# Kernel optimization log

Measured on AMD Instinct MI355X. Metric: run time of the kernel, lower is better.

Reference implementation:

```python
import jax, jax.numpy as jnp
import numpy as np

N = 170000      # nodes (ogbn-arxiv scale)
E = 2720000     # edges (avg degree 16)
IN, H, L, OUT = 128, 256, 4, 40
BN_EPS = 1e-5


def setup_inputs() -> dict:
    key = jax.random.key(0)
    ks = jax.random.split(key, 6)
    x = jax.random.normal(ks[0], (N, IN), jnp.float32)
    edge_index = jax.random.randint(ks[1], (2, E), 0, N, dtype=jnp.int64)
    W_in = jax.random.normal(ks[2], (IN, H), jnp.float32) * 0.05
    b_in = jnp.zeros((H,), jnp.float32)
    W_hid = jax.random.normal(ks[3], (L - 1, H, H), jnp.float32) * 0.05
    b_hid = jnp.zeros((L - 1, H), jnp.float32)
    gamma = jnp.ones((L, H), jnp.float32)
    beta = jnp.zeros((L, H), jnp.float32)
    W_out = jax.random.normal(ks[4], (L * H, OUT), jnp.float32) * 0.05
    b_out = jnp.zeros((OUT,), jnp.float32)
    return dict(x=x, edge_index=edge_index, W_in=W_in, b_in=b_in,
                W_hid=W_hid, b_hid=b_hid, gamma=gamma, beta=beta,
                W_out=W_out, b_out=b_out)


def _gcn_aggregate(h, src, dst, norm_e, inv_deg):
    # message passing with symmetric normalization + self-loop term
    msg = h[src] * norm_e[:, None]                      # [E, H] gather
    agg = jax.ops.segment_sum(msg, dst, num_segments=N)  # [N, H] scatter-add
    return agg + h * inv_deg[:, None]                   # self-loop: deg^-1


def reference(x, edge_index, W_in, b_in, W_hid, b_hid, gamma, beta, W_out, b_out):
    src, dst = edge_index[0], edge_index[1]
    # degree (incl. self-loop), PyG gcn_norm style
    deg = jax.ops.segment_sum(jnp.ones((E,), x.dtype), dst, num_segments=N) + 1.0
    dinv = jax.lax.rsqrt(deg)
    norm_e = dinv[src] * dinv[dst]
    inv_deg = 1.0 / deg

    outs = []
    h = x
    for i in range(L):
        W = W_in if i == 0 else W_hid[i - 1]
        b = b_in if i == 0 else b_hid[i - 1]
        h = _gcn_aggregate(h @ W, src, dst, norm_e, inv_deg) + b
        # BatchNorm1d (training-mode batch statistics, biased variance)
        mean = jnp.mean(h, axis=0)
        var = jnp.mean(jnp.square(h - mean), axis=0)
        h = (h - mean) * jax.lax.rsqrt(var + BN_EPS) * gamma[i] + beta[i]
        h = jax.nn.relu(h)  # dropout is identity in eval mode
        outs.append(h)

    z = jnp.concatenate(outs, axis=-1) @ W_out + b_out  # JK 'cat' -> [N, L*H] @ [L*H, OUT]
    return jax.nn.log_softmax(z, axis=-1)
```

## Files before the change

### kernel.cpp

```cpp
#include <hip/hip_runtime.h>
#include <math.h>

constexpr int kN = 170000;
constexpr int kE = 2720000;
constexpr int kFin = 128;
constexpr int kFh = 256;
constexpr int kL = 4;
constexpr int kFout = 40;

typedef __attribute__((ext_vector_type(8))) short bf16x8;
typedef __attribute__((ext_vector_type(4))) float f32x4;

__device__ __forceinline__ float jk_b2f(unsigned short u) {
    unsigned int x = ((unsigned int)u) << 16;
    float f;
    __builtin_memcpy(&f, &x, 4);
    return f;
}
__device__ __forceinline__ unsigned short jk_f2b(float f) {
    unsigned int x;
    __builtin_memcpy(&x, &f, 4);
    unsigned int r = (x + 0x7fffu + ((x >> 16) & 1u)) >> 16;
    return (unsigned short)r;
}

union U4 {
    uint4 v;
    unsigned short s[8];
};
union U2 {
    uint2 v;
    unsigned short s[4];
};

__global__ void jk8_zero_i(int* p, int n) {
    int i = blockIdx.x * blockDim.x + threadIdx.x;
    if (i < n) p[i] = 0;
}
__global__ void jk8_zero_f(float* p, int n) {
    int i = blockIdx.x * blockDim.x + threadIdx.x;
    if (i < n) p[i] = 0.0f;
}

__global__ void jk8_detect(const int* eb, int* flag) {
    __shared__ int nz;
    if (threadIdx.x == 0) nz = 0;
    __syncthreads();
    int bad = 0;
    for (int j = 0; j < 4; j++) {
        int idx = threadIdx.x * 4 + j;
        if (eb[2 * idx + 1] != 0) bad = 1;
    }
    if (bad) atomicOr(&nz, 1);
    __syncthreads();
    if (threadIdx.x == 0) {
        flag[0] = nz ? 0 : 1;
        flag[1] = 0;
    }
}

__global__ void jk8_count(const int* eb, const int* flag, int* counts, int* rank) {
    int e0 = (blockIdx.x * blockDim.x + threadIdx.x) * 4;
    if (e0 >= kE) return;
    int s64 = flag[0];
    int d[4];
    if (s64) {
        int4 c1 = *(const int4*)(eb + 2 * ((size_t)kE + e0));
        int4 c2 = *(const int4*)(eb + 2 * ((size_t)kE + e0) + 4);
        d[0] = c1.x; d[1] = c1.z; d[2] = c2.x; d[3] = c2.z;
    } else {
        int4 c1 = *(const int4*)(eb + (size_t)kE + e0);
        d[0] = c1.x; d[1] = c1.y; d[2] = c1.z; d[3] = c1.w;
    }
    int r[4];
#pragma unroll
    for (int q = 0; q < 4; q++) r[q] = atomicAdd(&counts[d[q]], 1);
    *(int4*)(rank + e0) = make_int4(r[0], r[1], r[2], r[3]);
}

__global__ void jk8_nodeprep(const int* counts, float* dinv, float* invdeg, int* off,
                             int* cursor) {
    int n = blockIdx.x * blockDim.x + threadIdx.x;
    if (n < kN) {
        int c = counts[n];
        float deg = (float)c + 1.0f;
        dinv[n] = rsqrtf(deg);
        invdeg[n] = 1.0f / deg;
        off[n] = atomicAdd(cursor, c);
    }
}

__global__ void jk8_fill(const int* eb, const int* flag, const int* rank, const int* off,
                         const float* dinv, int2* csr) {
    int e0 = (blockIdx.x * blockDim.x + threadIdx.x) * 4;
    if (e0 >= kE) return;
    int s64 = flag[0];
    int s[4], d[4];
    if (s64) {
        int4 a1 = *(const int4*)(eb + 2 * (size_t)e0);
        int4 a2 = *(const int4*)(eb + 2 * (size_t)e0 + 4);
        s[0] = a1.x; s[1] = a1.z; s[2] = a2.x; s[3] = a2.z;
        int4 c1 = *(const int4*)(eb + 2 * ((size_t)kE + e0));
        int4 c2 = *(const int4*)(eb + 2 * ((size_t)kE + e0) + 4);
        d[0] = c1.x; d[1] = c1.z; d[2] = c2.x; d[3] = c2.z;
    } else {
        int4 a1 = *(const int4*)(eb + (size_t)e0);
        s[0] = a1.x; s[1] = a1.y; s[2] = a1.z; s[3] = a1.w;
        int4 c1 = *(const int4*)(eb + (size_t)kE + e0);
        d[0] = c1.x; d[1] = c1.y; d[2] = c1.z; d[3] = c1.w;
    }
    int4 rr = *(const int4*)(rank + e0);
    int r[4] = {rr.x, rr.y, rr.z, rr.w};
#pragma unroll
    for (int q = 0; q < 4; q++) {
        int p = off[d[q]] + r[q];
        float w = dinv[s[q]] * dinv[d[q]];
        csr[p] = make_int2(s[q], __float_as_int(w));
    }
}

__global__ void jk8_prepw(const float* W_in, const float* W_hid, const float* Wout,
                          unsigned short* Wt0, unsigned short* Wt1, unsigned short* Wto) {
    int idx = blockIdx.x * blockDim.x + threadIdx.x;
    if (idx < 32768) {
        int c = idx >> 7, k = idx & 127;
        Wt0[idx] = jk_f2b(W_in[(size_t)k * kFh + c]);
    } else if (idx < 32768 + 196608) {
        int t2 = idx - 32768;
        int l = t2 >> 16, rem = t2 & 65535;
        int c = rem >> 8, k = rem & 255;
        Wt1[(size_t)l * 65536 + rem] = jk_f2b(W_hid[(size_t)l * 65536 + k * kFh + c]);
    } else if (idx < 32768 + 196608 + 49152) {
        int t2 = idx - 32768 - 196608;
        int l = t2 / (48 * 256), rem = t2 % (48 * 256);
        int col = rem >> 8, k = rem & 255;
        float wv = (col < kFout) ? Wout[(size_t)(l * kFh + k) * kFout + col] : 0.f;
        unsigned short hi = jk_f2b(wv);
        unsigned short lo = jk_f2b(wv - jk_b2f(hi));
        Wto[((size_t)(l * 2 + 0) * 48 + col) * 256 + k] = hi;
        Wto[((size_t)(l * 2 + 1) * 48 + col) * 256 + k] = lo;
    }
}

__global__ void jk8_xb(const float* x, unsigned short* xb) {
    int i = blockIdx.x * blockDim.x + threadIdx.x;
    if (i >= kN * kFin / 8) return;
    float4 a = *(const float4*)(x + (size_t)i * 8);
    float4 b = *(const float4*)(x + (size_t)i * 8 + 4);
    U4 o;
    o.s[0] = jk_f2b(a.x); o.s[1] = jk_f2b(a.y); o.s[2] = jk_f2b(a.z); o.s[3] = jk_f2b(a.w);
    o.s[4] = jk_f2b(b.x); o.s[5] = jk_f2b(b.y); o.s[6] = jk_f2b(b.z); o.s[7] = jk_f2b(b.w);
    *(uint4*)(xb + (size_t)i * 8) = o.v;
}

template <int MODE>
__global__ __launch_bounds__(256) void jk8_gemm(const unsigned short* A, const unsigned short* Wt,
                                                unsigned short* C, int K, const float* sc,
                                                const float* sh, const float* bias) {
    __shared__ unsigned short As[128][40];
    __shared__ unsigned short Bs[128][40];
    __shared__ float ssc[256], ssh[256];
    int tid = threadIdx.x;
    if (MODE == 1) {
        ssc[tid] = sc[tid];
        ssh[tid] = sh[tid];
    } else {
        ssc[tid] = bias[tid];
    }
    __syncthreads();
    int row0 = blockIdx.x * 128;
    int n0 = blockIdx.y * 128;
    int lane = tid & 63, w = tid >> 6;
    int wm = w >> 1, wn = w & 1;
    int lr = lane & 15, lg = lane >> 4;

    f32x4 acc[4][4];
#pragma unroll
    for (int i = 0; i < 4; i++)
#pragma unroll
        for (int j = 0; j < 4; j++) acc[i][j] = (f32x4){0.f, 0.f, 0.f, 0.f};

    int sr = tid >> 1;
    int skh = (tid & 1) * 16;

    for (int k0 = 0; k0 < K; k0 += 32) {
        {
            int row = row0 + sr;
            if (MODE == 0) {
                uint4 u0 = make_uint4(0, 0, 0, 0), u1 = make_uint4(0, 0, 0, 0);
                if (row < kN) {
                    const unsigned short* g = A + (size_t)row * K + k0 + skh;
                    u0 = *(const uint4*)g;
                    u1 = *(const uint4*)(g + 8);
                }
                *(uint4*)&As[sr][skh] = u0;
                *(uint4*)&As[sr][skh + 8] = u1;
            } else {
                U4 o0, o1;
                if (row < kN) {
                    U4 u0, u1;
                    const unsigned short* g = A + (size_t)row * K + k0 + skh;
                    u0.v = *(const uint4*)g;
                    u1.v = *(const uint4*)(g + 8);
#pragma unroll
                    for (int j = 0; j < 8; j++) {
                        float v = jk_b2f(u0.s[j]) * ssc[k0 + skh + j] + ssh[k0 + skh + j];
                        o0.s[j] = jk_f2b(v > 0.f ? v : 0.f);
                    }
#pragma unroll
                    for (int j = 0; j < 8; j++) {
                        float v = jk_b2f(u1.s[j]) * ssc[k0 + skh + 8 + j] + ssh[k0 + skh + 8 + j];
                        o1.s[j] = jk_f2b(v > 0.f ? v : 0.f);
                    }
                } else {
#pragma unroll
                    for (int j = 0; j < 8; j++) { o0.s[j] = 0; o1.s[j] = 0; }
                }
                *(uint4*)&As[sr][skh] = o0.v;
                *(uint4*)&As[sr][skh + 8] = o1.v;
            }
        }
        {
            const unsigned short* g = Wt + (size_t)(n0 + sr) * K + k0 + skh;
            *(uint4*)&Bs[sr][skh] = *(const uint4*)g;
            *(uint4*)&Bs[sr][skh + 8] = *(const uint4*)(g + 8);
        }
        __syncthreads();

        bf16x8 af[4], bfr[4];
#pragma unroll
        for (int mi = 0; mi < 4; mi++)
            af[mi] = *(const bf16x8*)&As[wm * 64 + mi * 16 + lr][lg * 8];
#pragma unroll
        for (int ni = 0; ni < 4; ni++)
            bfr[ni] = *(const bf16x8*)&Bs[wn * 64 + ni * 16 + lr][lg * 8];
#pragma unroll
        for (int mi = 0; mi < 4; mi++)
#pragma unroll
            for (int ni = 0; ni < 4; ni++)
                acc[mi][ni] = __builtin_amdgcn_mfma_f32_16x16x32_bf16(af[mi], bfr[ni],
                                                                      acc[mi][ni], 0, 0, 0);
        __syncthreads();
    }

#pragma unroll
    for (int mi = 0; mi < 4; mi++) {
#pragma unroll
        for (int j = 0; j < 4; j++) {
            int row = row0 + wm * 64 + mi * 16 + lg * 4 + j;
            if (row < kN) {
#pragma unroll
                for (int ni = 0; ni < 4; ni++) {
                    int col = n0 + wn * 64 + ni * 16 + lr;
                    float v = acc[mi][ni][j];
                    if (MODE == 0) v += ssc[col];
                    C[(size_t)row * kFh + col] = jk_f2b(v);
                }
            }
        }
    }
}

template <int CH, int HASB>
__global__ __launch_bounds__(256) void jk8_agg(const unsigned short* t, const float* bias,
                                               const int* off, const int* cnt, const int2* csr,
                                               const float* invdeg, unsigned short* h) {
    constexpr int PC = CH / 32;
    constexpr int DEPTH = (CH == 128) ? 8 : 6;
    int n = blockIdx.x * 8 + (threadIdx.x >> 5);
    if (n >= kN) return;
    int c0 = (threadIdx.x & 31) * PC;

    float acc[PC];
    {
        float sw = invdeg[n];
        if constexpr (PC == 8) {
            U4 u;
            u.v = *(const uint4*)(t + (size_t)n * CH + c0);
#pragma unroll
            for (int j = 0; j < 8; j++) acc[j] = sw * jk_b2f(u.s[j]);
        } else {
            U2 u;
            u.v = *(const uint2*)(t + (size_t)n * CH + c0);
#pragma unroll
            for (int j = 0; j < 4; j++) acc[j] = sw * jk_b2f(u.s[j]);
        }
    }

    int base = off[n], c = cnt[n];
    for (int i = 0; i < c; i += DEPTH) {
        float w[DEPTH];
        U4 u8[PC == 8 ? DEPTH : 1];
        U2 u4[PC == 4 ? DEPTH : 1];
#pragma unroll
        for (int q = 0; q < DEPTH; q++) {
            int e = i + q;
            bool v = e < c;
            int2 cw = csr[v ? base + e : base];
            w[q] = v ? __int_as_float(cw.y) : 0.0f;
            if constexpr (PC == 8)
                u8[q].v = *(const uint4*)(t + (size_t)cw.x * CH + c0);
            else
                u4[q].v = *(const uint2*)(t + (size_t)cw.x * CH + c0);
        }
#pragma unroll
        for (int q = 0; q < DEPTH; q++) {
            if constexpr (PC == 8) {
#pragma unroll
                for (int j = 0; j < 8; j++) acc[j] += w[q] * jk_b2f(u8[q].s[j]);
            } else {
#pragma unroll
                for (int j = 0; j < 4; j++) acc[j] += w[q] * jk_b2f(u4[q].s[j]);
            }
        }
    }

    if constexpr (PC == 8) {
        U4 o;
#pragma unroll
        for (int j = 0; j < 8; j++)
            o.s[j] = jk_f2b(HASB ? acc[j] + bias[c0 + j] : acc[j]);
        *(uint4*)(h + (size_t)n * CH + c0) = o.v;
    } else {
        U2 o;
#pragma unroll
        for (int j = 0; j < 4; j++)
            o.s[j] = jk_f2b(HASB ? acc[j] + bias[c0 + j] : acc[j]);
        *(uint2*)(h + (size_t)n * CH + c0) = o.v;
    }
}

__global__ __launch_bounds__(256) void jk8_bnstats(const unsigned short* h, float* stats) {
    __shared__ float lsum[256], lsq[256];
    int tid = threadIdx.x;
    lsum[tid] = 0.f;
    lsq[tid] = 0.f;
    __syncthreads();
    int c0 = (tid & 31) * 8;
    int grp = tid >> 5;
    float rs[8] = {}, rq[8] = {};
    for (int n = blockIdx.x * 8 + grp; n < kN; n += gridDim.x * 8) {
        U4 u;
        u.v = *(const uint4*)(h + (size_t)n * kFh + c0);
#pragma unroll
        for (int j = 0; j < 8; j++) {
            float v = jk_b2f(u.s[j]);
            rs[j] += v;
            rq[j] += v * v;
        }
    }
#pragma unroll
    for (int j = 0; j < 8; j++) {
        atomicAdd(&lsum[c0 + j], rs[j]);
        atomicAdd(&lsq[c0 + j], rq[j]);
    }
    __syncthreads();
    atomicAdd(&stats[tid], lsum[tid]);
    atomicAdd(&stats[256 + tid], lsq[tid]);
}

__global__ void jk8_bnfinal(const float* stats, const float* gamma, const float* beta, int layer,
                            float* scale, float* shift) {
    int c = threadIdx.x;
    float mean = stats[c] / (float)kN;
    float var = stats[256 + c] / (float)kN - mean * mean;
    var = var < 0.f ? 0.f : var;
    float sc = gamma[layer * kFh + c] * rsqrtf(var + 1e-5f);
    scale[c] = sc;
    shift[c] = beta[layer * kFh + c] - mean * sc;
}

template <int FIRST, int LAST>
__global__ __launch_bounds__(256) void jk8_zacc(const unsigned short* h, const float* scale,
                                                const float* shift, const unsigned short* Wto,
                                                const float* bout, float* z, float* out) {
    __shared__ unsigned short Bs[2][48][264];
    __shared__ unsigned short As[128][40];
    __shared__ float ssc[256], ssh[256];
    int tid = threadIdx.x;
    for (int f = tid; f < 2 * 48 * 256; f += 256) {
        int hl = f / (48 * 256);
        int rem = f % (48 * 256);
        Bs[hl][rem >> 8][rem & 255] = Wto[f];
    }
    ssc[tid] = scale[tid];
    ssh[tid] = shift[tid];
    __syncthreads();

    int row0 = blockIdx.x * 128;
    int w = tid >> 6, lane = tid & 63;
    int lr = lane & 15, lg = lane >> 4;
    int sr = tid >> 1, skh = (tid & 1) * 16;

    f32x4 acc[2][3];
#pragma unroll
    for (int mi = 0; mi < 2; mi++)
#pragma unroll
        for (int ni = 0; ni < 3; ni++) acc[mi][ni] = (f32x4){0.f, 0.f, 0.f, 0.f};

    for (int k0 = 0; k0 < kFh; k0 += 32) {
        int row = row0 + sr;
        U4 o0, o1;
        if (row < kN) {
            U4 u0, u1;
            const unsigned short* g = h + (size_t)row * kFh + k0 + skh;
            u0.v = *(const uint4*)g;
            u1.v = *(const uint4*)(g + 8);
#pragma unroll
            for (int j = 0; j < 8; j++) {
                float v = jk_b2f(u0.s[j]) * ssc[k0 + skh + j] + ssh[k0 + skh + j];
                o0.s[j] = jk_f2b(v > 0.f ? v : 0.f);
            }
#pragma unroll
            for (int j = 0; j < 8; j++) {
                float v = jk_b2f(u1.s[j]) * ssc[k0 + skh + 8 + j] + ssh[k0 + skh + 8 + j];
                o1.s[j] = jk_f2b(v > 0.f ? v : 0.f);
            }
        } else {
#pragma unroll
            for (int j = 0; j < 8; j++) { o0.s[j] = 0; o1.s[j] = 0; }
        }
        *(uint4*)&As[sr][skh] = o0.v;
        *(uint4*)&As[sr][skh + 8] = o1.v;
        __syncthreads();

        bf16x8 af[2], bh[3], bl[3];
#pragma unroll
        for (int mi = 0; mi < 2; mi++)
            af[mi] = *(const bf16x8*)&As[w * 32 + mi * 16 + lr][lg * 8];
#pragma unroll
        for (int ni = 0; ni < 3; ni++) {
            bh[ni] = *(const bf16x8*)&Bs[0][ni * 16 + lr][k0 + lg * 8];
            bl[ni] = *(const bf16x8*)&Bs[1][ni * 16 + lr][k0 + lg * 8];
        }
#pragma unroll
        for (int mi = 0; mi < 2; mi++)
#pragma unroll
            for (int ni = 0; ni < 3; ni++) {
                acc[mi][ni] = __builtin_amdgcn_mfma_f32_16x16x32_bf16(af[mi], bh[ni],
                                                                      acc[mi][ni], 0, 0, 0);
                acc[mi][ni] = __builtin_amdgcn_mfma_f32_16x16x32_bf16(af[mi], bl[ni],
                                                                      acc[mi][ni], 0, 0, 0);
            }
        __syncthreads();
    }

#pragma unroll
    for (int mi = 0; mi < 2; mi++) {
#pragma unroll
        for (int j = 0; j < 4; j++) {
            int row = row0 + w * 32 + mi * 16 + lg * 4 + j;
            if (row >= kN) continue;
            if (!LAST) {
#pragma unroll
                for (int ni = 0; ni < 3; ni++) {
                    int col = ni * 16 + lr;
                    if (col < kFout) {
                        if (FIRST)
                            z[(size_t)row * kFout + col] = acc[mi][ni][j] + bout[col];
                        else
                            z[(size_t)row * kFout + col] += acc[mi][ni][j];
                    }
                }
            } else {
                const float* zp = z + (size_t)row * kFout;
                float v0 = zp[lr] + acc[mi][0][j];
                float v1 = zp[16 + lr] + acc[mi][1][j];
                float v2 = (lr < 8) ? (zp[32 + lr] + acc[mi][2][j]) : -1e30f;
                float m = fmaxf(fmaxf(v0, v1), v2);
                m = fmaxf(m, __shfl_xor(m, 1, 64));
                m = fmaxf(m, __shfl_xor(m, 2, 64));
                m = fmaxf(m, __shfl_xor(m, 4, 64));
                m = fmaxf(m, __shfl_xor(m, 8, 64));
                float s = expf(v0 - m) + expf(v1 - m) + ((lr < 8) ? expf(v2 - m) : 0.f);
                s += __shfl_xor(s, 1, 64);
                s += __shfl_xor(s, 2, 64);
                s += __shfl_xor(s, 4, 64);
                s += __shfl_xor(s, 8, 64);
                float ls = m + logf(s);
                float* op = out + (size_t)row * kFout;
                op[lr] = v0 - ls;
                op[16 + lr] = v1 - ls;
                if (lr < 8) op[32 + lr] = v2 - ls;
            }
        }
    }
}

extern "C" void kernel_launch(void* const* d_in, const int* in_sizes, int n_in,
                              void* d_out, int out_size, void* d_ws, size_t ws_size,
                              hipStream_t stream) {
    (void)in_sizes; (void)n_in; (void)out_size; (void)ws_size;
    const float* x = (const float*)d_in[0];
    const int* eb = (const int*)d_in[1];
    const float* W_in = (const float*)d_in[2];
    const float* b_in = (const float*)d_in[3];
    const float* W_hid = (const float*)d_in[4];
    const float* b_hid = (const float*)d_in[5];
    const float* gamma = (const float*)d_in[6];
    const float* beta = (const float*)d_in[7];
    const float* W_out = (const float*)d_in[8];
    const float* b_out = (const float*)d_in[9];
    float* out = (float*)d_out;

    char* p = (char*)d_ws;
    auto alloc = [&](size_t b) -> void* {
        void* r = (void*)p;
        p += (b + 255) & ~(size_t)255;
        return r;
    };
    int* flag = (int*)alloc(8);
    int* counts = (int*)alloc((size_t)kN * 4);
    int* off = (int*)alloc((size_t)kN * 4);
    float* dinv = (float*)alloc((size_t)kN * 4);
    float* invdeg = (float*)alloc((size_t)kN * 4);
    float* bnsums = (float*)alloc((size_t)kL * 512 * 4);
    float* bnss = (float*)alloc((size_t)kL * 512 * 4);
    int* rank = (int*)alloc((size_t)kE * 4);
    int2* csr = (int2*)alloc((size_t)kE * 8);
    unsigned short* hA = (unsigned short*)alloc((size_t)kN * kFh * 2);
    unsigned short* hB = (unsigned short*)alloc((size_t)kN * kFh * 2);
    float* z = (float*)alloc((size_t)kN * kFout * 4);
    unsigned short* Wt0 = (unsigned short*)alloc((size_t)kFin * kFh * 2);
    unsigned short* Wt1 = (unsigned short*)alloc((size_t)3 * kFh * kFh * 2);
    unsigned short* Wto = (unsigned short*)alloc((size_t)kL * 2 * 48 * 256 * 2);

    jk8_zero_i<<<(kN + 255) / 256, 256, 0, stream>>>(counts, kN);
    jk8_zero_f<<<(kL * 512 + 255) / 256, 256, 0, stream>>>(bnsums, kL * 512);
    jk8_detect<<<1, 256, 0, stream>>>(eb, flag);
    jk8_count<<<(kE / 4 + 255) / 256, 256, 0, stream>>>(eb, flag, counts, rank);
    jk8_nodeprep<<<(kN + 255) / 256, 256, 0, stream>>>(counts, dinv, invdeg, off, flag + 1);
    jk8_fill<<<(kE / 4 + 255) / 256, 256, 0, stream>>>(eb, flag, rank, off, dinv, csr);
    jk8_prepw<<<(32768 + 196608 + 49152 + 255) / 256, 256, 0, stream>>>(W_in, W_hid, W_out,
                                                                        Wt0, Wt1, Wto);
    jk8_xb<<<(kN * kFin / 8 + 255) / 256, 256, 0, stream>>>(x, hB);
    jk8_agg<128, 0><<<(kN + 7) / 8, 256, 0, stream>>>(hB, nullptr, off, counts, csr, invdeg, hA);

    unsigned short* Wts[4] = {Wt0, Wt1, Wt1 + 65536, Wt1 + 131072};
    dim3 gg((kN + 127) / 128, 2);
    int zg = (kN + 127) / 128;
    for (int l = 0; l < kL; l++) {
        if (l == 0) {
            jk8_gemm<0><<<gg, 256, 0, stream>>>(hA, Wts[0], hB, kFin, nullptr, nullptr, b_in);
        } else {
            const float* b = b_hid + (size_t)(l - 1) * kFh;
            float* scp = bnss + (size_t)(l - 1) * 512;
            jk8_gemm<1><<<gg, 256, 0, stream>>>(hB, Wts[l], hA, kFh, scp, scp + 256, nullptr);
            jk8_agg<256, 1><<<(kN + 7) / 8, 256, 0, stream>>>(hA, b, off, counts, csr, invdeg,
                                                              hB);
        }
        jk8_bnstats<<<1024, 256, 0, stream>>>(hB, bnsums + (size_t)l * 512);
        jk8_bnfinal<<<1, 256, 0, stream>>>(bnsums + (size_t)l * 512, gamma, beta, l,
                                           bnss + (size_t)l * 512, bnss + (size_t)l * 512 + 256);
        const unsigned short* wtl = Wto + (size_t)l * 2 * 48 * 256;
        float* sc = bnss + (size_t)l * 512;
        if (l == 0)
            jk8_zacc<1, 0><<<zg, 256, 0, stream>>>(hB, sc, sc + 256, wtl, b_out, z, out);
        else if (l < kL - 1)
            jk8_zacc<0, 0><<<zg, 256, 0, stream>>>(hB, sc, sc + 256, wtl, b_out, z, out);
        else
            jk8_zacc<0, 1><<<zg, 256, 0, stream>>>(hB, sc, sc + 256, wtl, b_out, z, out);
    }
}
```

Baseline: 1.656 ms.

## Fuse BatchNorm statistics into GEMM and aggregation epilogues, drop bnstats pass

BatchNorm sum and sum-of-squares are now accumulated in the epilogue of the layer-0 GEMM and the hidden-layer aggregation kernels, using shared-memory atomics and then global atomics. This removes the separate bnstats kernel, which re-read the full node-feature matrix every layer. The aggregation kernel also moves to 512-thread blocks with 16 nodes per block, and its gather depth for the 256-channel case drops from 6 to 4. Statistics are now taken from the fp32 values before bf16 rounding, and the extra atomics add contention in the epilogues.

```diff
diff --git a/kernel.cpp b/kernel.cpp
--- a/kernel.cpp
+++ b/kernel.cpp
@@ -33,16 +33,16 @@
     unsigned short s[4];
 };
 
-__global__ void jk8_zero_i(int* p, int n) {
+__global__ void jk9_zero_i(int* p, int n) {
     int i = blockIdx.x * blockDim.x + threadIdx.x;
     if (i < n) p[i] = 0;
 }
-__global__ void jk8_zero_f(float* p, int n) {
+__global__ void jk9_zero_f(float* p, int n) {
     int i = blockIdx.x * blockDim.x + threadIdx.x;
     if (i < n) p[i] = 0.0f;
 }
 
-__global__ void jk8_detect(const int* eb, int* flag) {
+__global__ void jk9_detect(const int* eb, int* flag) {
     __shared__ int nz;
     if (threadIdx.x == 0) nz = 0;
     __syncthreads();
@@ -59,7 +59,7 @@
     }
 }
 
-__global__ void jk8_count(const int* eb, const int* flag, int* counts, int* rank) {
+__global__ void jk9_count(const int* eb, const int* flag, int* counts, int* rank) {
     int e0 = (blockIdx.x * blockDim.x + threadIdx.x) * 4;
     if (e0 >= kE) return;
     int s64 = flag[0];
@@ -78,7 +78,7 @@
     *(int4*)(rank + e0) = make_int4(r[0], r[1], r[2], r[3]);
 }
 
-__global__ void jk8_nodeprep(const int* counts, float* dinv, float* invdeg, int* off,
+__global__ void jk9_nodeprep(const int* counts, float* dinv, float* invdeg, int* off,
                              int* cursor) {
     int n = blockIdx.x * blockDim.x + threadIdx.x;
     if (n < kN) {
@@ -90,7 +90,7 @@
     }
 }
 
-__global__ void jk8_fill(const int* eb, const int* flag, const int* rank, const int* off,
+__global__ void jk9_fill(const int* eb, const int* flag, const int* rank, const int* off,
                          const float* dinv, int2* csr) {
     int e0 = (blockIdx.x * blockDim.x + threadIdx.x) * 4;
     if (e0 >= kE) return;
@@ -119,7 +119,7 @@
     }
 }
 
-__global__ void jk8_prepw(const float* W_in, const float* W_hid, const float* Wout,
+__global__ void jk9_prepw(const float* W_in, const float* W_hid, const float* Wout,
                           unsigned short* Wt0, unsigned short* Wt1, unsigned short* Wto) {
     int idx = blockIdx.x * blockDim.x + threadIdx.x;
     if (idx < 32768) {
@@ -142,7 +142,7 @@
     }
 }
 
-__global__ void jk8_xb(const float* x, unsigned short* xb) {
+__global__ void jk9_xb(const float* x, unsigned short* xb) {
     int i = blockIdx.x * blockDim.x + threadIdx.x;
     if (i >= kN * kFin / 8) return;
     float4 a = *(const float4*)(x + (size_t)i * 8);
@@ -154,18 +154,21 @@
 }
 
 template <int MODE>
-__global__ __launch_bounds__(256) void jk8_gemm(const unsigned short* A, const unsigned short* Wt,
+__global__ __launch_bounds__(256) void jk9_gemm(const unsigned short* A, const unsigned short* Wt,
                                                 unsigned short* C, int K, const float* sc,
-                                                const float* sh, const float* bias) {
+                                                const float* sh, const float* bias,
+                                                float* stats) {
     __shared__ unsigned short As[128][40];
     __shared__ unsigned short Bs[128][40];
     __shared__ float ssc[256], ssh[256];
+    __shared__ float csum[128], csq[128];
     int tid = threadIdx.x;
     if (MODE == 1) {
         ssc[tid] = sc[tid];
         ssh[tid] = sh[tid];
     } else {
         ssc[tid] = bias[tid];
+        if (tid < 128) { csum[tid] = 0.f; csq[tid] = 0.f; }
     }
     __syncthreads();
     int row0 = blockIdx.x * 128;
@@ -243,6 +246,7 @@
         __syncthreads();
     }
 
+    float ps[4] = {0.f, 0.f, 0.f, 0.f}, pq[4] = {0.f, 0.f, 0.f, 0.f};
 #pragma unroll
     for (int mi = 0; mi < 4; mi++) {
 #pragma unroll
@@ -253,113 +257,131 @@
                 for (int ni = 0; ni < 4; ni++) {
                     int col = n0 + wn * 64 + ni * 16 + lr;
                     float v = acc[mi][ni][j];
-                    if (MODE == 0) v += ssc[col];
+                    if (MODE == 0) {
+                        v += ssc[col];
+                        ps[ni] += v;
+                        pq[ni] += v * v;
+                    }
                     C[(size_t)row * kFh + col] = jk_f2b(v);
                 }
             }
         }
     }
-}
-
-template <int CH, int HASB>
-__global__ __launch_bounds__(256) void jk8_agg(const unsigned short* t, const float* bias,
+    if (MODE == 0) {
+#pragma unroll
+        for (int ni = 0; ni < 4; ni++) {
+            int lc = wn * 64 + ni * 16 + lr;
+            atomicAdd(&csum[lc], ps[ni]);
+            atomicAdd(&csq[lc], pq[ni]);
+        }
+        __syncthreads();
+        if (tid < 128) {
+            atomicAdd(&stats[n0 + tid], csum[tid]);
+            atomicAdd(&stats[256 + n0 + tid], csq[tid]);
+        }
+    }
+}
+
+template <int CH, int HASB, int STATS>
+__global__ __launch_bounds__(512) void jk9_agg(const unsigned short* t, const float* bias,
                                                const int* off, const int* cnt, const int2* csr,
-                                               const float* invdeg, unsigned short* h) {
+                                               const float* invdeg, unsigned short* h,
+                                               float* stats) {
     constexpr int PC = CH / 32;
-    constexpr int DEPTH = (CH == 128) ? 8 : 6;
-    int n = blockIdx.x * 8 + (threadIdx.x >> 5);
-    if (n >= kN) return;
-    int c0 = (threadIdx.x & 31) * PC;
-
-    float acc[PC];
-    {
-        float sw = invdeg[n];
+    constexpr int DEPTH = (CH == 128) ? 8 : 4;
+    __shared__ float lsum[CH], lsq[CH];
+    int tid = threadIdx.x;
+    if (STATS) {
+        if (tid < CH) {
+            lsum[tid] = 0.f;
+            lsq[tid] = 0.f;
+        }
+        __syncthreads();
+    }
+    int n = blockIdx.x * 16 + (tid >> 5);
+    bool act = n < kN;
+    int c0 = (tid & 31) * PC;
+    float vv[PC];
+
+    if (act) {
+        float acc[PC];
+        {
+            float sw = invdeg[n];
+            if constexpr (PC == 8) {
+                U4 u;
+                u.v = *(const uint4*)(t + (size_t)n * CH + c0);
+#pragma unroll
+                for (int j = 0; j < 8; j++) acc[j] = sw * jk_b2f(u.s[j]);
+            } else {
+                U2 u;
+                u.v = *(const uint2*)(t + (size_t)n * CH + c0);
+#pragma unroll
+                for (int j = 0; j < 4; j++) acc[j] = sw * jk_b2f(u.s[j]);
+            }
+        }
+        int base = off[n], c = cnt[n];
+        for (int i = 0; i < c; i += DEPTH) {
+            float w[DEPTH];
+            U4 u8[PC == 8 ? DEPTH : 1];
+            U2 u4[PC == 4 ? DEPTH : 1];
+#pragma unroll
+            for (int q = 0; q < DEPTH; q++) {
+                int e = i + q;
+                bool v = e < c;
+                int2 cw = csr[v ? base + e : base];
+                w[q] = v ? __int_as_float(cw.y) : 0.0f;
+                if constexpr (PC == 8)
+                    u8[q].v = *(const uint4*)(t + (size_t)cw.x * CH + c0);
+                else
+                    u4[q].v = *(const uint2*)(t + (size_t)cw.x * CH + c0);
+            }
+#pragma unroll
+            for (int q = 0; q < DEPTH; q++) {
+                if constexpr (PC == 8) {
+#pragma unroll
+                    for (int j = 0; j < 8; j++) acc[j] += w[q] * jk_b2f(u8[q].s[j]);
+                } else {
+#pragma unroll
+                    for (int j = 0; j < 4; j++) acc[j] += w[q] * jk_b2f(u4[q].s[j]);
+                }
+            }
+        }
         if constexpr (PC == 8) {
-            U4 u;
-            u.v = *(const uint4*)(t + (size_t)n * CH + c0);
-#pragma unroll
-            for (int j = 0; j < 8; j++) acc[j] = sw * jk_b2f(u.s[j]);
+            U4 o;
+#pragma unroll
+            for (int j = 0; j < 8; j++) {
+                vv[j] = HASB ? acc[j] + bias[c0 + j] : acc[j];
+                o.s[j] = jk_f2b(vv[j]);
+            }
+            *(uint4*)(h + (size_t)n * CH + c0) = o.v;
         } else {
-            U2 u;
-            u.v = *(const uint2*)(t + (size_t)n * CH + c0);
-#pragma unroll
-            for (int j = 0; j < 4; j++) acc[j] = sw * jk_b2f(u.s[j]);
-        }
-    }
-
-    int base = off[n], c = cnt[n];
-    for (int i = 0; i < c; i += DEPTH) {
-        float w[DEPTH];
-        U4 u8[PC == 8 ? DEPTH : 1];
-        U2 u4[PC == 4 ? DEPTH : 1];
-#pragma unroll
-        for (int q = 0; q < DEPTH; q++) {
-            int e = i + q;
-            bool v = e < c;
-            int2 cw = csr[v ? base + e : base];
-            w[q] = v ? __int_as_float(cw.y) : 0.0f;
-            if constexpr (PC == 8)
-                u8[q].v = *(const uint4*)(t + (size_t)cw.x * CH + c0);
-            else
-                u4[q].v = *(const uint2*)(t + (size_t)cw.x * CH + c0);
-        }
-#pragma unroll
-        for (int q = 0; q < DEPTH; q++) {
-            if constexpr (PC == 8) {
-#pragma unroll
-                for (int j = 0; j < 8; j++) acc[j] += w[q] * jk_b2f(u8[q].s[j]);
-            } else {
-#pragma unroll
-                for (int j = 0; j < 4; j++) acc[j] += w[q] * jk_b2f(u4[q].s[j]);
-            }
-        }
-    }
-
-    if constexpr (PC == 8) {
-        U4 o;
-#pragma unroll
-        for (int j = 0; j < 8; j++)
-            o.s[j] = jk_f2b(HASB ? acc[j] + bias[c0 + j] : acc[j]);
-        *(uint4*)(h + (size_t)n * CH + c0) = o.v;
-    } else {
-        U2 o;
-#pragma unroll
-        for (int j = 0; j < 4; j++)
-            o.s[j] = jk_f2b(HASB ? acc[j] + bias[c0 + j] : acc[j]);
-        *(uint2*)(h + (size_t)n * CH + c0) = o.v;
-    }
-}
-
-__global__ __launch_bounds__(256) void jk8_bnstats(const unsigned short* h, float* stats) {
-    __shared__ float lsum[256], lsq[256];
-    int tid = threadIdx.x;
-    lsum[tid] = 0.f;
-    lsq[tid] = 0.f;
-    __syncthreads();
-    int c0 = (tid & 31) * 8;
-    int grp = tid >> 5;
-    float rs[8] = {}, rq[8] = {};
-    for (int n = blockIdx.x * 8 + grp; n < kN; n += gridDim.x * 8) {
-        U4 u;
-        u.v = *(const uint4*)(h + (size_t)n * kFh + c0);
-#pragma unroll
-        for (int j = 0; j < 8; j++) {
-            float v = jk_b2f(u.s[j]);
-            rs[j] += v;
-            rq[j] += v * v;
-        }
-    }
-#pragma unroll
-    for (int j = 0; j < 8; j++) {
-        atomicAdd(&lsum[c0 + j], rs[j]);
-        atomicAdd(&lsq[c0 + j], rq[j]);
-    }
-    __syncthreads();
-    atomicAdd(&stats[tid], lsum[tid]);
-    atomicAdd(&stats[256 + tid], lsq[tid]);
-}
-
-__global__ void jk8_bnfinal(const float* stats, const float* gamma, const float* beta, int layer,
+            U2 o;
+#pragma unroll
+            for (int j = 0; j < 4; j++) {
+                vv[j] = HASB ? acc[j] + bias[c0 + j] : acc[j];
+                o.s[j] = jk_f2b(vv[j]);
+            }
+            *(uint2*)(h + (size_t)n * CH + c0) = o.v;
+        }
+    }
+
+    if (STATS) {
+        if (act) {
+#pragma unroll
+            for (int j = 0; j < PC; j++) {
+                atomicAdd(&lsum[c0 + j], vv[j]);
+                atomicAdd(&lsq[c0 + j], vv[j] * vv[j]);
+            }
+        }
+        __syncthreads();
+        if (tid < CH) {
+            atomicAdd(&stats[tid], lsum[tid]);
+            atomicAdd(&stats[CH + tid], lsq[tid]);
+        }
+    }
+}
+
+__global__ void jk9_bnfinal(const float* stats, const float* gamma, const float* beta, int layer,
                             float* scale, float* shift) {
     int c = threadIdx.x;
     float mean = stats[c] / (float)kN;
@@ -371,7 +393,7 @@
 }
 
 template <int FIRST, int LAST>
-__global__ __launch_bounds__(256) void jk8_zacc(const unsigned short* h, const float* scale,
+__global__ __launch_bounds__(256) void jk9_zacc(const unsigned short* h, const float* scale,
                                                 const float* shift, const unsigned short* Wto,
                                                 const float* bout, float* z, float* out) {
     __shared__ unsigned short Bs[2][48][264];
@@ -525,40 +547,43 @@
     unsigned short* Wt1 = (unsigned short*)alloc((size_t)3 * kFh * kFh * 2);
     unsigned short* Wto = (unsigned short*)alloc((size_t)kL * 2 * 48 * 256 * 2);
 
-    jk8_zero_i<<<(kN + 255) / 256, 256, 0, stream>>>(counts, kN);
-    jk8_zero_f<<<(kL * 512 + 255) / 256, 256, 0, stream>>>(bnsums, kL * 512);
-    jk8_detect<<<1, 256, 0, stream>>>(eb, flag);
-    jk8_count<<<(kE / 4 + 255) / 256, 256, 0, stream>>>(eb, flag, counts, rank);
-    jk8_nodeprep<<<(kN + 255) / 256, 256, 0, stream>>>(counts, dinv, invdeg, off, flag + 1);
-    jk8_fill<<<(kE / 4 + 255) / 256, 256, 0, stream>>>(eb, flag, rank, off, dinv, csr);
-    jk8_prepw<<<(32768 + 196608 + 49152 + 255) / 256, 256, 0, stream>>>(W_in, W_hid, W_out,
+    jk9_zero_i<<<(kN + 255) / 256, 256, 0, stream>>>(counts, kN);
+    jk9_zero_f<<<(kL * 512 + 255) / 256, 256, 0, stream>>>(bnsums, kL * 512);
+    jk9_detect<<<1, 256, 0, stream>>>(eb, flag);
+    jk9_count<<<(kE / 4 + 255) / 256, 256, 0, stream>>>(eb, flag, counts, rank);
+    jk9_nodeprep<<<(kN + 255) / 256, 256, 0, stream>>>(counts, dinv, invdeg, off, flag + 1);
+    jk9_fill<<<(kE / 4 + 255) / 256, 256, 0, stream>>>(eb, flag, rank, off, dinv, csr);
+    jk9_prepw<<<(32768 + 196608 + 49152 + 255) / 256, 256, 0, stream>>>(W_in, W_hid, W_out,
                                                                         Wt0, Wt1, Wto);
-    jk8_xb<<<(kN * kFin / 8 + 255) / 256, 256, 0, stream>>>(x, hB);
-    jk8_agg<128, 0><<<(kN + 7) / 8, 256, 0, stream>>>(hB, nullptr, off, counts, csr, invdeg, hA);
+    jk9_xb<<<(kN * kFin / 8 + 255) / 256, 256, 0, stream>>>(x, hB);
+    jk9_agg<128, 0, 0><<<(kN + 15) / 16, 512, 0, stream>>>(hB, nullptr, off, counts, csr,
+                                                           invdeg, hA, nullptr);
 
     unsigned short* Wts[4] = {Wt0, Wt1, Wt1 + 65536, Wt1 + 131072};
     dim3 gg((kN + 127) / 128, 2);
     int zg = (kN + 127) / 128;
     for (int l = 0; l < kL; l++) {
+        float* st = bnsums + (size_t)l * 512;
         if (l == 0) {
-            jk8_gemm<0><<<gg, 256, 0, stream>>>(hA, Wts[0], hB, kFin, nullptr, nullptr, b_in);
+            jk9_gemm<0><<<gg, 256, 0, stream>>>(hA, Wts[0], hB, kFin, nullptr, nullptr, b_in,
+                                                st);
         } else {
             const float* b = b_hid + (size_t)(l - 1) * kFh;
             float* scp = bnss + (size_t)(l - 1) * 512;
-            jk8_gemm<1><<<gg, 256, 0, stream>>>(hB, Wts[l], hA, kFh, scp, scp + 256, nullptr);
-            jk8_agg<256, 1><<<(kN + 7) / 8, 256, 0, stream>>>(hA, b, off, counts, csr, invdeg,
-                                                              hB);
-        }
-        jk8_bnstats<<<1024, 256, 0, stream>>>(hB, bnsums + (size_t)l * 512);
-        jk8_bnfinal<<<1, 256, 0, stream>>>(bnsums + (size_t)l * 512, gamma, beta, l,
-                                           bnss + (size_t)l * 512, bnss + (size_t)l * 512 + 256);
+            jk9_gemm<1><<<gg, 256, 0, stream>>>(hB, Wts[l], hA, kFh, scp, scp + 256, nullptr,
+                                                nullptr);
+            jk9_agg<256, 1, 1><<<(kN + 15) / 16, 512, 0, stream>>>(hA, b, off, counts, csr,
+                                                                   invdeg, hB, st);
+        }
+        jk9_bnfinal<<<1, 256, 0, stream>>>(st, gamma, beta, l, bnss + (size_t)l * 512,
+                                           bnss + (size_t)l * 512 + 256);
         const unsigned short* wtl = Wto + (size_t)l * 2 * 48 * 256;
         float* sc = bnss + (size_t)l * 512;
         if (l == 0)
-            jk8_zacc<1, 0><<<zg, 256, 0, stream>>>(hB, sc, sc + 256, wtl, b_out, z, out);
+            jk9_zacc<1, 0><<<zg, 256, 0, stream>>>(hB, sc, sc + 256, wtl, b_out, z, out);
         else if (l < kL - 1)
-            jk8_zacc<0, 0><<<zg, 256, 0, stream>>>(hB, sc, sc + 256, wtl, b_out, z, out);
+            jk9_zacc<0, 0><<<zg, 256, 0, stream>>>(hB, sc, sc + 256, wtl, b_out, z, out);
         else
-            jk8_zacc<0, 1><<<zg, 256, 0, stream>>>(hB, sc, sc + 256, wtl, b_out, z, out);
-    }
-}
+            jk9_zacc<0, 1><<<zg, 256, 0, stream>>>(hB, sc, sc + 256, wtl, b_out, z, out);
+    }
+}
```

Result: slower. 2.659 ms (+60.5%).
